# Performance work log

Hardware: AMD Instinct MI355X
Metric: run time of the kernel (lower is better)

The kernel has to match this reference:

```python
import jax, jax.numpy as jnp
import numpy as np

B, S, D, H = 2, 2048, 1024, 16
HD = D // H  # head dim = 64

def setup_inputs() -> dict:
    key = jax.random.key(0)
    k1, k2, k3, k4, k5 = jax.random.split(key, 5)
    return {
        "x": jax.random.normal(k1, (B, S, D), dtype=jnp.float32),
        "w_qkv": jax.random.normal(k2, (D, 3 * D), dtype=jnp.float32) * (1.0 / np.sqrt(D)),
        "b_qkv": jax.random.normal(k3, (3 * D,), dtype=jnp.float32) * 0.02,
        "w_out": jax.random.normal(k4, (D, D), dtype=jnp.float32) * (1.0 / np.sqrt(D)),
        "b_out": jax.random.normal(k5, (D,), dtype=jnp.float32) * 0.02,
        "c": 0,
    }

def reference(x, w_qkv, b_qkv, w_out, b_out, c):
    # fused QKV projection: [B,S,3D]
    qkv = jnp.einsum('bsd,de->bse', x, w_qkv) + b_qkv
    q, k, v = jnp.split(qkv, 3, axis=-1)
    # [B,S,D] -> [B,H,S,HD]
    split_heads = lambda t: t.reshape(B, S, H, HD).transpose(0, 2, 1, 3)
    q, k, v = split_heads(q), split_heads(k), split_heads(v)
    scale = 1.0 / np.sqrt(HD).astype(np.float32)
    scores = jnp.einsum('bhqd,bhkd->bhqk', q, k) * scale  # [B,H,S,S]
    probs = jax.nn.softmax(scores, axis=-1)
    # c==1 noise path references an undefined `const` in the original (dead/broken);
    # dropout probs are 0 -> identity (eval mode).
    attn = jnp.einsum('bhqk,bhkd->bhqd', probs, v)  # [B,H,S,HD]
    attn = attn.transpose(0, 2, 1, 3).reshape(B, S, D)
    out = jnp.einsum('bsd,de->bse', attn, w_out) + b_out
    return out
```

## Files before the change

### kernel.cpp

```cpp
#include <hip/hip_runtime.h>


typedef __attribute__((ext_vector_type(8))) short bs8;
typedef __attribute__((ext_vector_type(4))) short bs4;
typedef __attribute__((ext_vector_type(4))) float f32x4;
typedef __attribute__((ext_vector_type(16))) float f32x16;

#define QSCALE 0.18033688011112042f
#define MBOUND 24.0f

__device__ __forceinline__ unsigned short f2bf(float f) {
  union { float f; unsigned int u; } v; v.f = f;
  return (unsigned short)((v.u + 0x8000u) >> 16);
}

__device__ __forceinline__ unsigned int pkbf2(float a, float b) {
  union { float f; unsigned int u; } va, vb; va.f = a; vb.f = b;
#if defined(__HIP_DEVICE_COMPILE__)
  return __builtin_amdgcn_perm(vb.u + 0x8000u, va.u + 0x8000u, 0x07060302u);
#else
  return 0u;
#endif
}

__device__ __forceinline__ void pls32(unsigned int &a, unsigned int &b) {
#if defined(__HIP_DEVICE_COMPILE__)
  asm("v_permlane32_swap_b32 %0, %1" : "+v"(a), "+v"(b));
#endif
}

__device__ __forceinline__ void async16(const unsigned short* g, unsigned short* lds) {
  __builtin_amdgcn_global_load_lds(
      (const __attribute__((address_space(1))) unsigned int*)g,
      (__attribute__((address_space(3))) unsigned int*)lds, 16, 0, 0);
}

__device__ __forceinline__ void stage_rows64(unsigned short* lds, const unsigned short* src,
                                             int ldk, int w, int l) {
#pragma unroll
  for (int i = 0; i < 4; ++i) {
    int row = (w * 4 + i) * 8 + (l >> 3);
    int cg  = (l & 7) ^ (l >> 3);
    async16(src + (size_t)row * ldk + cg * 8, lds + (w * 4 + i) * 512);
  }
}

__device__ __forceinline__ void stage_rows64_8w(unsigned short* lds, const unsigned short* src,
                                                int ldk, int w, int l) {
#pragma unroll
  for (int i = 0; i < 2; ++i) {
    int row = (w * 2 + i) * 8 + (l >> 3);
    int cg  = (l & 7) ^ (l >> 3);
    async16(src + (size_t)row * ldk + cg * 8, lds + (w * 2 + i) * 512);
  }
}

__device__ __forceinline__ void stage_vt_8w(unsigned short* lds, const unsigned short* vtb,
                                            int keyofs, int w, int l) {
#pragma unroll
  for (int i = 0; i < 2; ++i) {
    int row = (w * 2 + i) * 4 + (l >> 4);
    int cg = (l & 15) ^ (row & 15);
    async16(vtb + (size_t)row * 2048 + keyofs + cg * 8, lds + (w * 2 + i) * 512);
  }
}

__device__ __forceinline__ void transpose_cast_body(const float* __restrict__ src,
                                                    unsigned short* __restrict__ dst,
                                                    int R, int C, int bx, int by, int t) {
  __shared__ unsigned short tile[64][73];
  int c0 = bx * 64, r0 = by * 64;
  int rl = t >> 2, cb = (t & 3) * 16;
  const float* p = src + (size_t)(r0 + rl) * C + c0 + cb;
#pragma unroll
  for (int j = 0; j < 16; j += 4) {
    float4 f = *(const float4*)(p + j);
    tile[rl][cb + j + 0] = f2bf(f.x);
    tile[rl][cb + j + 1] = f2bf(f.y);
    tile[rl][cb + j + 2] = f2bf(f.z);
    tile[rl][cb + j + 3] = f2bf(f.w);
  }
  __syncthreads();
  int cl = t >> 2, rb = (t & 3) * 16;
  unsigned short* q = dst + (size_t)(c0 + cl) * R + r0 + rb;
#pragma unroll
  for (int j = 0; j < 16; ++j) q[j] = tile[rb + j][cl];
}

__global__ __launch_bounds__(256) void prep_kernel(const float* __restrict__ x,
                                                   unsigned short* __restrict__ xb,
                                                   const float* __restrict__ w_qkv,
                                                   unsigned short* __restrict__ wt1,
                                                   const float* __restrict__ w_out,
                                                   unsigned short* __restrict__ wt2) {
  int blk = blockIdx.x, t = threadIdx.x;
  if (blk < 2048) {
    int i = (blk * 256 + t) * 8;
    float4 a = *(const float4*)(x + i);
    float4 b = *(const float4*)(x + i + 4);
    union { bs8 v; unsigned short u[8]; } o;
    o.u[0] = f2bf(a.x); o.u[1] = f2bf(a.y); o.u[2] = f2bf(a.z); o.u[3] = f2bf(a.w);
    o.u[4] = f2bf(b.x); o.u[5] = f2bf(b.y); o.u[6] = f2bf(b.z); o.u[7] = f2bf(b.w);
    *(bs8*)(xb + i) = o.v;
  } else if (blk < 2816) {
    int i = blk - 2048;
    transpose_cast_body(w_qkv, wt1, 1024, 3072, i % 48, i / 48, t);
  } else {
    int i = blk - 2816;
    transpose_cast_body(w_out, wt2, 1024, 1024, i % 16, i / 16, t);
  }
}

__global__ __launch_bounds__(256) void gemm_qkv_kernel(const unsigned short* __restrict__ A,
                                                       const unsigned short* __restrict__ Bt,
                                                       const float* __restrict__ bias,
                                                       unsigned short* __restrict__ qo,
                                                       unsigned short* __restrict__ ko,
                                                       unsigned short* __restrict__ vto) {
  __shared__ unsigned short As[128 * 64];
  __shared__ unsigned short Bs[128 * 64];
  int t = threadIdx.x, w = t >> 6, l = t & 63;
  int m16 = l & 15, q = l >> 4;
  int wm = w >> 1, wn = w & 1;
  int bm = blockIdx.y, bn = blockIdx.x;
  bool vsec = (bn >= 16);
  const unsigned short* Abase = A + (size_t)bm * 128 * 1024;
  const unsigned short* Bbase = Bt + (size_t)bn * 128 * 1024;
  f32x4 zero4 = {0.f, 0.f, 0.f, 0.f};
  f32x4 acc[4][4];
#pragma unroll
  for (int i = 0; i < 4; ++i)
#pragma unroll
    for (int j = 0; j < 4; ++j) acc[i][j] = zero4;
  for (int kt = 0; kt < 16; ++kt) {
    stage_rows64(As, Abase + kt * 64, 1024, w, l);
    stage_rows64(Bs, Bbase + kt * 64, 1024, w, l);
    __syncthreads();
#pragma unroll
    for (int ks = 0; ks < 2; ++ks) {
      bs8 af[4], bf[4];
#pragma unroll
      for (int mt = 0; mt < 4; ++mt) {
        int row = wm * 64 + mt * 16 + m16;
        int c = ks * 4 + q;
        af[mt] = *(const bs8*)&As[row * 64 + ((c ^ (row & 7)) * 8)];
      }
#pragma unroll
      for (int nt = 0; nt < 4; ++nt) {
        int row = wn * 64 + nt * 16 + m16;
        int c = ks * 4 + q;
        bf[nt] = *(const bs8*)&Bs[row * 64 + ((c ^ (row & 7)) * 8)];
      }
      if (vsec) {
#pragma unroll
        for (int mt = 0; mt < 4; ++mt)
#pragma unroll
          for (int nt = 0; nt < 4; ++nt)
            acc[mt][nt] = __builtin_amdgcn_mfma_f32_16x16x32_bf16(af[mt], bf[nt],
                                                                  acc[mt][nt], 0, 0, 0);
      } else {
#pragma unroll
        for (int mt = 0; mt < 4; ++mt)
#pragma unroll
          for (int nt = 0; nt < 4; ++nt)
            acc[mt][nt] = __builtin_amdgcn_mfma_f32_16x16x32_bf16(bf[nt], af[mt],
                                                                  acc[mt][nt], 0, 0, 0);
      }
    }
    __syncthreads();
  }
  if (!vsec) {
#pragma unroll
    for (int nt = 0; nt < 4; ++nt) {
      int ng0 = bn * 128 + wn * 64 + nt * 16 + q * 4;
      float4 bb = *(const float4*)&bias[ng0];
      int sect = ng0 >> 10;
      unsigned short* dst = sect ? ko : qo;
      float sc = sect ? 1.0f : QSCALE;
      int f0 = ng0 & 1023, h = f0 >> 6, hd0 = f0 & 63;
#pragma unroll
      for (int mt = 0; mt < 4; ++mt) {
        int mg = bm * 128 + wm * 64 + mt * 16 + m16;
        int b = mg >> 11, s = mg & 2047;
        union { bs4 v; unsigned short u[4]; } pv;
        pv.u[0] = f2bf((acc[mt][nt][0] + bb.x) * sc);
        pv.u[1] = f2bf((acc[mt][nt][1] + bb.y) * sc);
        pv.u[2] = f2bf((acc[mt][nt][2] + bb.z) * sc);
        pv.u[3] = f2bf((acc[mt][nt][3] + bb.w) * sc);
        *(bs4*)&dst[((size_t)(b * 16 + h) * 2048 + s) * 64 + hd0] = pv.v;
      }
    }
  } else {
#pragma unroll
    for (int nt = 0; nt < 4; ++nt) {
      int ng = bn * 128 + wn * 64 + nt * 16 + m16;
      float bb = bias[ng];
      int f = ng & 1023, h = f >> 6, hd = f & 63;
#pragma unroll
      for (int mt = 0; mt < 4; ++mt) {
        int mg0 = bm * 128 + wm * 64 + mt * 16 + q * 4;
        int b = mg0 >> 11, s0 = mg0 & 2047;
        union { bs4 v; unsigned short u[4]; } pv;
#pragma unroll
        for (int r = 0; r < 4; ++r) pv.u[r] = f2bf(acc[mt][nt][r] + bb);
        *(bs4*)&vto[((size_t)(b * 16 + h) * 64 + hd) * 2048 + s0] = pv.v;
      }
    }
  }
}

__global__ __launch_bounds__(256) void gemm_out_kernel(const unsigned short* __restrict__ A,
                                                       const unsigned short* __restrict__ Bt,
                                                       const float* __restrict__ bias,
                                                       float* __restrict__ out) {
  __shared__ unsigned short As[64 * 64];
  __shared__ unsigned short Bs[128 * 64];
  int t = threadIdx.x, w = t >> 6, l = t & 63;
  int m16 = l & 15, q = l >> 4;
  int wm = w >> 1, wn = w & 1;
  int bm = blockIdx.y, bn = blockIdx.x;
  const unsigned short* Abase = A + (size_t)bm * 64 * 1024;
  const unsigned short* Bbase = Bt + (size_t)bn * 128 * 1024;
  f32x4 zero4 = {0.f, 0.f, 0.f, 0.f};
  f32x4 acc[2][4];
#pragma unroll
  for (int i = 0; i < 2; ++i)
#pragma unroll
    for (int j = 0; j < 4; ++j) acc[i][j] = zero4;
  for (int kt = 0; kt < 16; ++kt) {
    stage_rows64_8w(As, Abase + kt * 64, 1024, w, l);
    stage_rows64(Bs, Bbase + kt * 64, 1024, w, l);
    __syncthreads();
#pragma unroll
    for (int ks = 0; ks < 2; ++ks) {
      bs8 af[2], bf[4];
#pragma unroll
      for (int mt = 0; mt < 2; ++mt) {
        int row = wm * 32 + mt * 16 + m16;
        int c = ks * 4 + q;
        af[mt] = *(const bs8*)&As[row * 64 + ((c ^ (row & 7)) * 8)];
      }
#pragma unroll
      for (int nt = 0; nt < 4; ++nt) {
        int row = wn * 64 + nt * 16 + m16;
        int c = ks * 4 + q;
        bf[nt] = *(const bs8*)&Bs[row * 64 + ((c ^ (row & 7)) * 8)];
      }
#pragma unroll
      for (int mt = 0; mt < 2; ++mt)
#pragma unroll
        for (int nt = 0; nt < 4; ++nt)
          acc[mt][nt] = __builtin_amdgcn_mfma_f32_16x16x32_bf16(bf[nt], af[mt],
                                                                acc[mt][nt], 0, 0, 0);
    }
    __syncthreads();
  }
#pragma unroll
  for (int nt = 0; nt < 4; ++nt) {
    int ng0 = bn * 128 + wn * 64 + nt * 16 + q * 4;
    float4 bb = *(const float4*)&bias[ng0];
#pragma unroll
    for (int mt = 0; mt < 2; ++mt) {
      int mg = bm * 64 + wm * 32 + mt * 16 + m16;
      float4 ov;
      ov.x = acc[mt][nt][0] + bb.x;
      ov.y = acc[mt][nt][1] + bb.y;
      ov.z = acc[mt][nt][2] + bb.z;
      ov.w = acc[mt][nt][3] + bb.w;
      *(float4*)&out[(size_t)mg * 1024 + ng0] = ov;
    }
  }
}

__global__ __launch_bounds__(512, 4) void attn_kernel(const unsigned short* __restrict__ Q,
                                                      const unsigned short* __restrict__ K,
                                                      const unsigned short* __restrict__ Vt,
                                                      unsigned short* __restrict__ Aout) {
  __shared__ unsigned short Ks[2][128 * 64];
  __shared__ unsigned short Vts[2][64 * 128];
  int t = threadIdx.x, w = t >> 6, l = t & 63;
  int c32 = l & 31, lh = l >> 5;
  int wq = w & 3, kh = w >> 2;
  int qt = blockIdx.x, bh = blockIdx.y;
  const unsigned short* qbase = Q + (size_t)bh * 2048 * 64 + (size_t)qt * 128 * 64;
  const unsigned short* kbase = K + (size_t)bh * 2048 * 64;
  const unsigned short* vtbase = Vt + (size_t)bh * 64 * 2048;

  bs8 qf[4];
#pragma unroll
  for (int ks = 0; ks < 4; ++ks)
    qf[ks] = *(const bs8*)(qbase + (size_t)(wq * 32 + c32) * 64 + ks * 16 + lh * 8);

  stage_rows64_8w(&Ks[0][0], kbase, 64, w, l);
  stage_vt_8w(&Vts[0][0], vtbase, 0, w, l);
  __syncthreads();

  f32x16 sAcc[2];
  f32x16 o[2];
  float lsum = 0.f;
#pragma unroll
  for (int nh = 0; nh < 2; ++nh)
#pragma unroll
    for (int r = 0; r < 16; ++r) o[nh][r] = 0.f;

  for (int kt = 0; kt < 16; ++kt) {
    int buf = kt & 1;
    if (kt < 15) {
      stage_rows64_8w(&Ks[buf ^ 1][0], kbase + (size_t)(kt + 1) * 128 * 64, 64, w, l);
      stage_vt_8w(&Vts[buf ^ 1][0], vtbase, (kt + 1) * 128, w, l);
    }
    const unsigned short* Kb = &Ks[buf][0];
    const unsigned short* Vb = &Vts[buf][0];

#pragma unroll
    for (int tile = 0; tile < 2; ++tile)
#pragma unroll
      for (int r = 0; r < 16; ++r) sAcc[tile][r] = -MBOUND;
#pragma unroll
    for (int ks = 0; ks < 4; ++ks) {
      int row0 = kh * 64 + c32;
      int row1 = row0 + 32;
      int cgr = ks * 2 + lh;
      bs8 kf0 = *(const bs8*)&Kb[row0 * 64 + ((cgr ^ (row0 & 7)) * 8)];
      bs8 kf1 = *(const bs8*)&Kb[row1 * 64 + ((cgr ^ (row1 & 7)) * 8)];
      __builtin_amdgcn_s_setprio(1);
      sAcc[0] = __builtin_amdgcn_mfma_f32_32x32x16_bf16(kf0, qf[ks], sAcc[0], 0, 0, 0);
      sAcc[1] = __builtin_amdgcn_mfma_f32_32x32x16_bf16(kf1, qf[ks], sAcc[1], 0, 0, 0);
      __builtin_amdgcn_s_setprio(0);
    }

#pragma unroll
    for (int tile = 0; tile < 2; ++tile) {
      float rs = 0.f;
      unsigned int wp[8];
#pragma unroll
      for (int ri = 0; ri < 8; ++ri) {
        float p0 = __builtin_amdgcn_exp2f(sAcc[tile][2 * ri]);
        float p1 = __builtin_amdgcn_exp2f(sAcc[tile][2 * ri + 1]);
        rs += p0 + p1;
        wp[ri] = pkbf2(p0, p1);
      }
      lsum += rs;
#pragma unroll
      for (int kp = 0; kp < 2; ++kp) {
        int ks2 = tile * 2 + kp;
        unsigned int W0 = wp[kp * 4 + 0], W2 = wp[kp * 4 + 2];
        unsigned int W1 = wp[kp * 4 + 1], W3 = wp[kp * 4 + 3];
        pls32(W0, W2);
        pls32(W1, W3);
        union { bs8 v; unsigned int u[4]; } pf;
        pf.u[0] = W0; pf.u[1] = W1; pf.u[2] = W2; pf.u[3] = W3;
        __builtin_amdgcn_s_setprio(1);
#pragma unroll
        for (int nh = 0; nh < 2; ++nh) {
          int vrow = nh * 32 + c32;
          int gk = kh * 8 + ks2 * 2 + lh;
          bs8 vf = *(const bs8*)&Vb[vrow * 128 + ((gk ^ (vrow & 15)) * 8)];
          o[nh] = __builtin_amdgcn_mfma_f32_32x32x16_bf16(vf, pf.v, o[nh], 0, 0, 0);
        }
        __builtin_amdgcn_s_setprio(0);
      }
    }
    __syncthreads();
  }

  float* ored = (float*)&Ks[0][0];
  float* lred = (float*)&Vts[0][0];
  if (kh == 1) {
#pragma unroll
    for (int nh = 0; nh < 2; ++nh)
#pragma unroll
      for (int c = 0; c < 4; ++c) {
        f32x4 t4 = { o[nh][c * 4 + 0], o[nh][c * 4 + 1],
                     o[nh][c * 4 + 2], o[nh][c * 4 + 3] };
        *(f32x4*)&ored[((nh * 4 + c) * 256 + wq * 64 + l) * 4] = t4;
      }
    lred[wq * 64 + l] = lsum;
  }
  __syncthreads();
  if (kh == 0) {
#pragma unroll
    for (int nh = 0; nh < 2; ++nh)
#pragma unroll
      for (int c = 0; c < 4; ++c) {
        f32x4 part = *(const f32x4*)&ored[((nh * 4 + c) * 256 + wq * 64 + l) * 4];
#pragma unroll
        for (int r = 0; r < 4; ++r) o[nh][c * 4 + r] += part[r];
      }
    lsum += lred[wq * 64 + l];

    float l0 = lsum;
    l0 += __shfl_xor(l0, 32);
    float inv = 1.0f / l0;

    int b = bh >> 4, hh = bh & 15;
    int s = qt * 128 + wq * 32 + c32;
#pragma unroll
    for (int nh = 0; nh < 2; ++nh)
#pragma unroll
      for (int rg = 0; rg < 4; ++rg) {
        union { bs4 v; unsigned short u[4]; } pv;
#pragma unroll
        for (int r = 0; r < 4; ++r) pv.u[r] = f2bf(o[nh][rg * 4 + r] * inv);
        int hd0 = nh * 32 + rg * 8 + 4 * lh;
        *(bs4*)&Aout[((size_t)(b * 2048 + s)) * 1024 + hh * 64 + hd0] = pv.v;
      }
  }
}

extern "C" void kernel_launch(void* const* d_in, const int* in_sizes, int n_in,
                              void* d_out, int out_size, void* d_ws, size_t ws_size,
                              hipStream_t stream) {
  const float* x     = (const float*)d_in[0];
  const float* w_qkv = (const float*)d_in[1];
  const float* b_qkv = (const float*)d_in[2];
  const float* w_out = (const float*)d_in[3];
  const float* b_out = (const float*)d_in[4];
  float* out = (float*)d_out;

  char* ws = (char*)d_ws;
  unsigned short* xb    = (unsigned short*)(ws);
  unsigned short* wt1   = (unsigned short*)(ws + (8u << 20));
  unsigned short* wt2   = (unsigned short*)(ws + (14u << 20));
  unsigned short* qb    = (unsigned short*)(ws + (16u << 20));
  unsigned short* kb    = (unsigned short*)(ws + (24u << 20));
  unsigned short* vtb   = (unsigned short*)(ws + (32u << 20));
  unsigned short* attnb = (unsigned short*)(ws + (40u << 20));

  prep_kernel<<<3072, 256, 0, stream>>>(x, xb, w_qkv, wt1, w_out, wt2);
  gemm_qkv_kernel<<<dim3(24, 32), 256, 0, stream>>>(xb, wt1, b_qkv, qb, kb, vtb);
  attn_kernel<<<dim3(16, 32), 512, 0, stream>>>(qb, kb, vtb, attnb);
  gemm_out_kernel<<<dim3(8, 64), 256, 0, stream>>>(attnb, wt2, b_out, out);
}
```

Baseline: 194.1 us.

## Compute softmax row sums via MFMA with ones, use hardware bf16 pack, stage output via LDS

Replaces the per-lane scalar accumulation of exp values with an extra MFMA that multiplies the packed probabilities by a ones vector, so the row sum comes out of the matrix unit and the cross-lane shuffle is no longer needed. It also swaps the manual round-and-permute bf16 packing for the v_cvt_pk_bf16_f32 instruction, and unrolls the key-tile loop by two. The final output is written into swizzled LDS first and then stored with 16-byte coalesced writes instead of scattered 8-byte stores. The costs are one extra MFMA per P·V step, an extra barrier, and a row sum taken from bf16-rounded probabilities, which changes rounding slightly.

New measurement: 227.5 us. +17.2%, slower.

```diff
diff --git a/kernel.cpp b/kernel.cpp
--- a/kernel.cpp
+++ b/kernel.cpp
@@ -14,10 +14,11 @@
   return (unsigned short)((v.u + 0x8000u) >> 16);
 }
 
-__device__ __forceinline__ unsigned int pkbf2(float a, float b) {
-  union { float f; unsigned int u; } va, vb; va.f = a; vb.f = b;
+__device__ __forceinline__ unsigned int cvtpk(float a, float b) {
 #if defined(__HIP_DEVICE_COMPILE__)
-  return __builtin_amdgcn_perm(vb.u + 0x8000u, va.u + 0x8000u, 0x07060302u);
+  unsigned int r;
+  asm("v_cvt_pk_bf16_f32 %0, %1, %2" : "=v"(r) : "v"(a), "v"(b));
+  return r;
 #else
   return 0u;
 #endif
@@ -291,18 +292,21 @@
   for (int ks = 0; ks < 4; ++ks)
     qf[ks] = *(const bs8*)(qbase + (size_t)(wq * 32 + c32) * 64 + ks * 16 + lh * 8);
 
+  union { bs8 v; unsigned short u[8]; } ones;
+#pragma unroll
+  for (int i = 0; i < 8; ++i) ones.u[i] = 0x3F80;
+
   stage_rows64_8w(&Ks[0][0], kbase, 64, w, l);
   stage_vt_8w(&Vts[0][0], vtbase, 0, w, l);
   __syncthreads();
 
   f32x16 sAcc[2];
   f32x16 o[2];
-  float lsum = 0.f;
-#pragma unroll
-  for (int nh = 0; nh < 2; ++nh)
-#pragma unroll
-    for (int r = 0; r < 16; ++r) o[nh][r] = 0.f;
-
+  f32x16 o2;
+#pragma unroll
+  for (int r = 0; r < 16; ++r) { o[0][r] = 0.f; o[1][r] = 0.f; o2[r] = 0.f; }
+
+#pragma unroll 2
   for (int kt = 0; kt < 16; ++kt) {
     int buf = kt & 1;
     if (kt < 15) {
@@ -331,16 +335,13 @@
 
 #pragma unroll
     for (int tile = 0; tile < 2; ++tile) {
-      float rs = 0.f;
       unsigned int wp[8];
 #pragma unroll
       for (int ri = 0; ri < 8; ++ri) {
         float p0 = __builtin_amdgcn_exp2f(sAcc[tile][2 * ri]);
         float p1 = __builtin_amdgcn_exp2f(sAcc[tile][2 * ri + 1]);
-        rs += p0 + p1;
-        wp[ri] = pkbf2(p0, p1);
-      }
-      lsum += rs;
+        wp[ri] = cvtpk(p0, p1);
+      }
 #pragma unroll
       for (int kp = 0; kp < 2; ++kp) {
         int ks2 = tile * 2 + kp;
@@ -358,6 +359,7 @@
           bs8 vf = *(const bs8*)&Vb[vrow * 128 + ((gk ^ (vrow & 15)) * 8)];
           o[nh] = __builtin_amdgcn_mfma_f32_32x32x16_bf16(vf, pf.v, o[nh], 0, 0, 0);
         }
+        o2 = __builtin_amdgcn_mfma_f32_32x32x16_bf16(ones.v, pf.v, o2, 0, 0, 0);
         __builtin_amdgcn_s_setprio(0);
       }
     }
@@ -365,7 +367,9 @@
   }
 
   float* ored = (float*)&Ks[0][0];
-  float* lred = (float*)&Vts[0][0];
+  float* lred = (float*)&Vts[1][0];
+  unsigned short* ot = &Vts[0][0];
+  int b = bh >> 4, hh = bh & 15;
   if (kh == 1) {
 #pragma unroll
     for (int nh = 0; nh < 2; ++nh)
@@ -375,7 +379,7 @@
                      o[nh][c * 4 + 2], o[nh][c * 4 + 3] };
         *(f32x4*)&ored[((nh * 4 + c) * 256 + wq * 64 + l) * 4] = t4;
       }
-    lred[wq * 64 + l] = lsum;
+    lred[wq * 64 + l] = o2[0];
   }
   __syncthreads();
   if (kh == 0) {
@@ -387,24 +391,28 @@
 #pragma unroll
         for (int r = 0; r < 4; ++r) o[nh][c * 4 + r] += part[r];
       }
-    lsum += lred[wq * 64 + l];
-
-    float l0 = lsum;
-    l0 += __shfl_xor(l0, 32);
-    float inv = 1.0f / l0;
-
-    int b = bh >> 4, hh = bh & 15;
-    int s = qt * 128 + wq * 32 + c32;
+    float lt = o2[0] + lred[wq * 64 + l];
+    float inv = 1.0f / lt;
+
+    int token = wq * 32 + c32;
 #pragma unroll
     for (int nh = 0; nh < 2; ++nh)
 #pragma unroll
       for (int rg = 0; rg < 4; ++rg) {
-        union { bs4 v; unsigned short u[4]; } pv;
-#pragma unroll
-        for (int r = 0; r < 4; ++r) pv.u[r] = f2bf(o[nh][rg * 4 + r] * inv);
-        int hd0 = nh * 32 + rg * 8 + 4 * lh;
-        *(bs4*)&Aout[((size_t)(b * 2048 + s)) * 1024 + hh * 64 + hd0] = pv.v;
-      }
+        union { bs4 v; unsigned int u[2]; } pv;
+        pv.u[0] = cvtpk(o[nh][rg * 4 + 0] * inv, o[nh][rg * 4 + 1] * inv);
+        pv.u[1] = cvtpk(o[nh][rg * 4 + 2] * inv, o[nh][rg * 4 + 3] * inv);
+        int g = nh * 4 + rg;
+        *(bs4*)&ot[token * 64 + ((g ^ (token & 7)) * 8) + lh * 4] = pv.v;
+      }
+  }
+  __syncthreads();
+#pragma unroll
+  for (int ps = 0; ps < 2; ++ps) {
+    int idx = ps * 512 + t;
+    int token = idx >> 3, g = idx & 7;
+    bs8 val = *(const bs8*)&ot[token * 64 + ((g ^ (token & 7)) * 8)];
+    *(bs8*)&Aout[((size_t)(b * 2048 + qt * 128 + token)) * 1024 + hh * 64 + g * 8] = val;
   }
 }
 
```
